# Kernel optimization log

Measured on AMD Instinct MI355X. Metric: run time of the kernel, lower is better.

Reference implementation:

```python
import math
import jax, jax.numpy as jnp
import numpy as np

EMBED_DIM = 768
NUM_HEADS = 12
HEAD_DIM = EMBED_DIM // NUM_HEADS
NUM_BUCKETS = 32
MAX_DISTANCE = 128
B, S = 8, 1024


def setup_inputs() -> dict:
    key = jax.random.key(0)
    ks = jax.random.split(key, 16)
    sc = 0.02
    d = {
        "query": jax.random.normal(ks[0], (B, S, EMBED_DIM), jnp.float32),
        "Wq": jax.random.normal(ks[1], (EMBED_DIM, EMBED_DIM), jnp.float32) * sc,
        "bq": jnp.zeros((EMBED_DIM,), jnp.float32),
        "Wk": jax.random.normal(ks[2], (EMBED_DIM, EMBED_DIM), jnp.float32) * sc,
        "bk": jnp.zeros((EMBED_DIM,), jnp.float32),
        "Wv": jax.random.normal(ks[3], (EMBED_DIM, EMBED_DIM), jnp.float32) * sc,
        "bv": jnp.zeros((EMBED_DIM,), jnp.float32),
        "Wo": jax.random.normal(ks[4], (EMBED_DIM, EMBED_DIM), jnp.float32) * sc,
        "bo": jnp.zeros((EMBED_DIM,), jnp.float32),
        "rel_embed": jax.random.normal(ks[5], (NUM_BUCKETS, NUM_HEADS), jnp.float32) * sc,
        "gru_W": jax.random.normal(ks[6], (HEAD_DIM, 8), jnp.float32) * sc,
        "gru_b": jnp.zeros((8,), jnp.float32),
        "gru_const": jnp.ones((1, NUM_HEADS, 1, 1), jnp.float32),
    }
    return d


def _rel_pos_bias(rel_embed, seq_len):
    # bidirectional T5-style bucketing, matching WavLM._relative_positions_bucket
    ctx = jnp.arange(seq_len)[:, None]
    mem = jnp.arange(seq_len)[None, :]
    rp = mem - ctx  # [S, S]
    nb = NUM_BUCKETS // 2
    buckets = (rp > 0).astype(jnp.int32) * nb
    arp = jnp.abs(rp)
    max_exact = nb // 2
    is_small = arp < max_exact
    # truncation toward zero == astype for positive values; clamp to avoid log(0)
    large = max_exact + (
        jnp.log(jnp.maximum(arp, 1).astype(jnp.float32) / max_exact)
        / math.log(MAX_DISTANCE / max_exact)
        * (nb - max_exact)
    ).astype(jnp.int32)
    large = jnp.minimum(large, nb - 1)
    buckets = buckets + jnp.where(is_small, arp, large)
    # embedding lookup -> [S, S, H] -> [H, S, S]
    return rel_embed[buckets].transpose(2, 0, 1)


def reference(query, Wq, bq, Wk, bk, Wv, bv, Wo, bo, rel_embed, gru_W, gru_b, gru_const):
    b, s, e = query.shape
    h, d = NUM_HEADS, HEAD_DIM
    pos_bias = _rel_pos_bias(rel_embed, s)  # [H, S, S]

    # GRU-style gate computed from raw query, per head
    ql = query.reshape(b, s, h, d).transpose(0, 2, 1, 3)  # [B, H, S, D]
    g = jax.nn.sigmoid((ql @ gru_W + gru_b).reshape(b, h, s, 2, 4).sum(-1))  # [B,H,S,2]
    gate_a = g[..., 0:1]
    gate_b = g[..., 1:2]
    gate = gate_a * (gate_b * gru_const - 1.0) + 2.0  # [B, H, S, 1]
    attn_mask = gate * pos_bias[None]  # [B, H, S, S]

    scale = d ** (-0.5)
    q = (query @ Wq + bq).reshape(b, s, h, d).transpose(0, 2, 1, 3) * scale
    k = (query @ Wk + bk).reshape(b, s, h, d).transpose(0, 2, 1, 3)
    v = (query @ Wv + bv).reshape(b, s, h, d).transpose(0, 2, 1, 3)

    scores = jnp.einsum("bhqd,bhkd->bhqk", q, k) + attn_mask
    w = jax.nn.softmax(scores, axis=-1)  # max-subtraction in torch is a no-op math-wise
    out = jnp.einsum("bhqk,bhkd->bhqd", w, v)
    out = out.transpose(0, 2, 1, 3).reshape(b, s, h * d)
    return out @ Wo + bo
```

## Files before the change

### kernel.cpp

```cpp
#include <hip/hip_runtime.h>
#include <hip/hip_bf16.h>
#include <math.h>

#define EMBED 768
#define NH 12
#define HD 64
#define SEQ 1024
#define BATCH 8
#define NROWS (BATCH * SEQ)
#define LOG2E 1.44269504088896340736f

typedef __attribute__((ext_vector_type(4))) float f32x4;
typedef __attribute__((ext_vector_type(8))) short short8;
typedef __attribute__((ext_vector_type(8))) _Float16 half8;
typedef unsigned short u16;

__device__ __forceinline__ u16 f2bf(float x) {
    union { float f; unsigned u; } v; v.f = x;
    unsigned r = v.u + 0x7fff + ((v.u >> 16) & 1);
    return (u16)(r >> 16);
}
__device__ __forceinline__ void split2h(float x, u16& hi, u16& lo) {
    _Float16 h = (_Float16)x;
    _Float16 l = (_Float16)(x - (float)h);
    union { _Float16 f; u16 u; } a, b;
    a.f = h; b.f = l;
    hi = a.u; lo = b.u;
}
__device__ __forceinline__ u16 f2h(float x) {
    union { _Float16 f; u16 u; } a; a.f = (_Float16)x; return a.u;
}
__device__ __forceinline__ unsigned pkbf(float a, float b) {
    union { __hip_bfloat162 v; unsigned u; } cv;
    cv.v = __float22bfloat162_rn(make_float2(a, b));
    return cv.u;
}
__device__ __forceinline__ void gll16(const void* g, void* l) {
    __builtin_amdgcn_global_load_lds(
        (const __attribute__((address_space(1))) unsigned int*)g,
        (__attribute__((address_space(3))) unsigned int*)l,
        16, 0, 0);
}

__global__ void bias_table_kernel(const float* __restrict__ rel_embed,
                                  float* __restrict__ bt)
{
    int idx = blockIdx.x * 256 + threadIdx.x;
    const int total = NH * 2047;
    if (idx >= total) return;
    int h    = idx / 2047;
    int dpos = idx - h * 2047;
    int rp   = dpos - 1023;
    int bucket = (rp > 0) ? 16 : 0;
    int arp = rp < 0 ? -rp : rp;
    if (arp < 8) {
        bucket += arp;
    } else {
        double v = log((double)arp / 8.0) / log(16.0) * 8.0;
        int l = 8 + (int)v;
        if (l > 15) l = 15;
        bucket += l;
    }
    bt[idx] = rel_embed[bucket * NH + h] * LOG2E;
}

__global__ void gate_kernel(const float* __restrict__ query,
                            const float* __restrict__ gru_W,
                            const float* __restrict__ gru_b,
                            const float* __restrict__ gru_c,
                            float* __restrict__ gate)
{
    int idx = blockIdx.x * 256 + threadIdx.x;
    if (idx >= BATCH * NH * SEQ) return;
    int s  = idx & (SEQ - 1);
    int bh = idx >> 10;
    int h  = bh % NH;
    int b  = bh / NH;

    const float* x = query + ((size_t)(b * SEQ + s) * EMBED + h * HD);
    float z[8] = {0.f, 0.f, 0.f, 0.f, 0.f, 0.f, 0.f, 0.f};
    for (int d = 0; d < HD; ++d) {
        float xv = x[d];
        const float* wrow = gru_W + d * 8;
        #pragma unroll
        for (int c = 0; c < 8; ++c) z[c] += xv * wrow[c];
    }
    float s0 = (z[0] + gru_b[0]) + (z[1] + gru_b[1]) + (z[2] + gru_b[2]) + (z[3] + gru_b[3]);
    float s1 = (z[4] + gru_b[4]) + (z[5] + gru_b[5]) + (z[6] + gru_b[6]) + (z[7] + gru_b[7]);
    float g0 = 1.f / (1.f + expf(-s0));
    float g1 = 1.f / (1.f + expf(-s1));
    gate[idx] = g0 * (g1 * gru_c[h] - 1.f) + 2.f;
}

__global__ __launch_bounds__(256)
void convertA_h(const float* __restrict__ A, u16* __restrict__ Ah,
                u16* __restrict__ Al)
{
    int idx = (blockIdx.x * 256 + threadIdx.x) * 4;
    float4 v = *(const float4*)(A + idx);
    ushort4 h, l;
    split2h(v.x, h.x, l.x); split2h(v.y, h.y, l.y);
    split2h(v.z, h.z, l.z); split2h(v.w, h.w, l.w);
    *(ushort4*)(Ah + idx) = h;
    *(ushort4*)(Al + idx) = l;
}

__global__ __launch_bounds__(256)
void convertWT_h(const float* __restrict__ W, u16* __restrict__ WT)
{
    __shared__ float tile[32][33];
    int t  = threadIdx.x;
    int k0 = blockIdx.y * 32, n0 = blockIdx.x * 32;
    int r = t >> 3, c = (t & 7) * 4;
    float4 v = *(const float4*)&W[(size_t)(k0 + r) * EMBED + n0 + c];
    tile[r][c] = v.x; tile[r][c + 1] = v.y; tile[r][c + 2] = v.z; tile[r][c + 3] = v.w;
    __syncthreads();
    int n = t >> 3, ks = (t & 7) * 4;
    ushort4 h;
    h.x = f2h(tile[ks    ][n]);
    h.y = f2h(tile[ks + 1][n]);
    h.z = f2h(tile[ks + 2][n]);
    h.w = f2h(tile[ks + 3][n]);
    *(ushort4*)&WT[(size_t)(n0 + n) * EMBED + k0 + ks] = h;
}

__global__ __launch_bounds__(256)
void gemm_qkv(const u16* __restrict__ Ah, const u16* __restrict__ Al,
              const u16* __restrict__ WqT, const u16* __restrict__ WkT,
              const u16* __restrict__ WvT,
              const float* __restrict__ bq, const float* __restrict__ bk,
              const float* __restrict__ bv,
              u16* __restrict__ Qb, u16* __restrict__ Kb, u16* __restrict__ VT,
              float qscale)
{
    __shared__ u16 Ah_s[32 * 32];
    __shared__ u16 Al_s[32 * 32];
    __shared__ u16 Bq_s[128 * 32];
    __shared__ u16 Bk_s[128 * 32];
    __shared__ u16 Bv_s[128 * 32];

    const int t    = threadIdx.x;
    const int lane = t & 63;
    const int wid  = t >> 6;
    const int L    = lane & 15;
    const int quad = lane >> 4;
    const int row0 = blockIdx.y * 32;
    const int col0 = blockIdx.x * 128;
    const int wm   = (wid >> 1) * 16;
    const int wn   = (wid & 1) * 64;

    f32x4 accQ[4], accK[4], accV[4];
    #pragma unroll
    for (int nt = 0; nt < 4; ++nt) {
        accQ[nt] = (f32x4){0.f, 0.f, 0.f, 0.f};
        accK[nt] = (f32x4){0.f, 0.f, 0.f, 0.f};
        accV[nt] = (f32x4){0.f, 0.f, 0.f, 0.f};
    }

    const int rA = (wid & 1) * 16 + (lane >> 2);
    const int cA = (lane & 3) ^ (rA & 3);
    const u16* gA = ((wid < 2) ? Ah : Al) + (size_t)(row0 + rA) * EMBED + 8 * cA;
    char* lA = (char*)((wid < 2) ? Ah_s : Al_s) + (wid & 1) * 1024;

    const int rB = t >> 2;
    const int cB = (t & 3) ^ (rB & 3);
    const size_t bo0 = (size_t)(col0 + rB) * EMBED + 8 * cB;
    const size_t bo1 = (size_t)(col0 + 64 + rB) * EMBED + 8 * cB;
    char* lBq = (char*)Bq_s + wid * 1024;
    char* lBk = (char*)Bk_s + wid * 1024;
    char* lBv = (char*)Bv_s + wid * 1024;

    const int swz = 8 * (quad ^ (L & 3));

    for (int k0 = 0; k0 < EMBED; k0 += 32) {
        __syncthreads();
        gll16(gA + k0, lA);
        gll16(WqT + bo0 + k0, lBq); gll16(WqT + bo1 + k0, lBq + 4096);
        gll16(WkT + bo0 + k0, lBk); gll16(WkT + bo1 + k0, lBk + 4096);
        gll16(WvT + bo0 + k0, lBv); gll16(WvT + bo1 + k0, lBv + 4096);
        __syncthreads();

        half8 ah = *(const half8*)&Ah_s[(wm + L) * 32 + swz];
        half8 al = *(const half8*)&Al_s[(wm + L) * 32 + swz];
        #pragma unroll
        for (int nt = 0; nt < 4; ++nt) {
            const int boff = (wn + nt * 16 + L) * 32 + swz;
            half8 b0 = *(const half8*)&Bq_s[boff];
            accQ[nt] = __builtin_amdgcn_mfma_f32_16x16x32_f16(ah, b0, accQ[nt], 0, 0, 0);
            accQ[nt] = __builtin_amdgcn_mfma_f32_16x16x32_f16(al, b0, accQ[nt], 0, 0, 0);
            half8 b1 = *(const half8*)&Bk_s[boff];
            accK[nt] = __builtin_amdgcn_mfma_f32_16x16x32_f16(ah, b1, accK[nt], 0, 0, 0);
            accK[nt] = __builtin_amdgcn_mfma_f32_16x16x32_f16(al, b1, accK[nt], 0, 0, 0);
            half8 b2 = *(const half8*)&Bv_s[boff];
            accV[nt] = __builtin_amdgcn_mfma_f32_16x16x32_f16(ah, b2, accV[nt], 0, 0, 0);
            accV[nt] = __builtin_amdgcn_mfma_f32_16x16x32_f16(al, b2, accV[nt], 0, 0, 0);
        }
    }

    float bq4[4], bk4[4], bv4[4];
    #pragma unroll
    for (int nt = 0; nt < 4; ++nt) {
        int n = col0 + wn + nt * 16 + L;
        bq4[nt] = bq[n]; bk4[nt] = bk[n]; bv4[nt] = bv[n];
    }

    const int rowa = row0 + wm + quad * 4;
    #pragma unroll
    for (int r = 0; r < 4; ++r) {
        size_t base = (size_t)(rowa + r) * EMBED + col0 + wn + L;
        #pragma unroll
        for (int nt = 0; nt < 4; ++nt) {
            Qb[base + nt * 16] = f2bf((accQ[nt][r] + bq4[nt]) * qscale);
            Kb[base + nt * 16] = f2bf(accK[nt][r] + bk4[nt]);
        }
    }
    {
        int b_  = rowa >> 10;
        int s0_ = rowa & 1023;
        #pragma unroll
        for (int nt = 0; nt < 4; ++nt) {
            int n = col0 + wn + nt * 16 + L;
            int hh = n >> 6, dd = n & 63;
            ushort4 pk;
            pk.x = f2bf(accV[nt][0] + bv4[nt]);
            pk.y = f2bf(accV[nt][1] + bv4[nt]);
            pk.z = f2bf(accV[nt][2] + bv4[nt]);
            pk.w = f2bf(accV[nt][3] + bv4[nt]);
            *(ushort4*)&VT[((size_t)(b_ * NH + hh) * HD + dd) * SEQ + s0_] = pk;
        }
    }
}

__global__ __launch_bounds__(256)
void gemm_out(const u16* __restrict__ Ah, const u16* __restrict__ Al,
              const u16* __restrict__ BT, const float* __restrict__ bias,
              float* __restrict__ C)
{
    __shared__ u16 Ah_s[32 * 32];
    __shared__ u16 Al_s[32 * 32];
    __shared__ u16 B_s[128 * 32];

    const int t    = threadIdx.x;
    const int lane = t & 63;
    const int wid  = t >> 6;
    const int L    = lane & 15;
    const int quad = lane >> 4;
    const int row0 = blockIdx.y * 32;
    const int col0 = blockIdx.x * 128;
    const int wm   = (wid >> 1) * 16;
    const int wn   = (wid & 1) * 64;

    f32x4 acc[4];
    #pragma unroll
    for (int nt = 0; nt < 4; ++nt) acc[nt] = (f32x4){0.f, 0.f, 0.f, 0.f};

    const int rA = (wid & 1) * 16 + (lane >> 2);
    const int cA = (lane & 3) ^ (rA & 3);
    const u16* gA = ((wid < 2) ? Ah : Al) + (size_t)(row0 + rA) * EMBED + 8 * cA;
    char* lA = (char*)((wid < 2) ? Ah_s : Al_s) + (wid & 1) * 1024;

    const int rB = t >> 2;
    const int cB = (t & 3) ^ (rB & 3);
    const u16* gB0 = BT + (size_t)(col0 + rB) * EMBED + 8 * cB;
    const u16* gB1 = BT + (size_t)(col0 + 64 + rB) * EMBED + 8 * cB;
    char* lB = (char*)B_s + wid * 1024;

    const int swz = 8 * (quad ^ (L & 3));

    for (int k0 = 0; k0 < EMBED; k0 += 32) {
        __syncthreads();
        gll16(gA  + k0, lA);
        gll16(gB0 + k0, lB);
        gll16(gB1 + k0, lB + 4096);
        __syncthreads();

        half8 ah = *(const half8*)&Ah_s[(wm + L) * 32 + swz];
        half8 al = *(const half8*)&Al_s[(wm + L) * 32 + swz];
        #pragma unroll
        for (int nt = 0; nt < 4; ++nt) {
            half8 b = *(const half8*)&B_s[(wn + nt * 16 + L) * 32 + swz];
            acc[nt] = __builtin_amdgcn_mfma_f32_16x16x32_f16(ah, b, acc[nt], 0, 0, 0);
            acc[nt] = __builtin_amdgcn_mfma_f32_16x16x32_f16(al, b, acc[nt], 0, 0, 0);
        }
    }

    float b4[4];
    #pragma unroll
    for (int nt = 0; nt < 4; ++nt) b4[nt] = bias[col0 + wn + nt * 16 + L];
    #pragma unroll
    for (int r = 0; r < 4; ++r) {
        size_t base = (size_t)(row0 + wm + quad * 4 + r) * EMBED + col0 + wn + L;
        #pragma unroll
        for (int nt = 0; nt < 4; ++nt)
            C[base + nt * 16] = acc[nt][r] + b4[nt];
    }
}

__global__ __launch_bounds__(256)
void attn_mfma3(const u16* __restrict__ Qg, const u16* __restrict__ Kg,
                const u16* __restrict__ VTg, const float* __restrict__ gate,
                const float* __restrict__ bias_tab,
                u16* __restrict__ Oh, u16* __restrict__ Ol)
{
    __shared__ float2   btP[2047];
    __shared__ u16      Klds[64 * 64];
    __shared__ u16      Vlds[64 * 64];
    __shared__ unsigned PB[4][32 * 20];

    const int t    = threadIdx.x;
    const int lane = t & 63;
    const int wid  = t >> 6;
    const int L    = lane & 15;
    const int quad = lane >> 4;

    const int bh = blockIdx.y;
    const int b  = bh / NH;
    const int h  = bh % NH;
    const int qw = blockIdx.x * 128 + wid * 32;

    for (int i = t; i < 2047; i += 256) {
        float a  = bias_tab[h * 2047 + i];
        float nb = (i < 2046) ? bias_tab[h * 2047 + i + 1] : 0.f;
        btP[i] = make_float2(a, nb);
    }

    short8 qf[2][2];
    int   qabs[2];
    float g2[2];
    #pragma unroll
    for (int qt = 0; qt < 2; ++qt) {
        qabs[qt] = qw + qt * 16 + L;
        g2[qt]   = gate[(size_t)bh * SEQ + qabs[qt]];
        const u16* qp = Qg + ((size_t)(b * SEQ + qabs[qt]) * EMBED + h * HD + quad * 8);
        qf[qt][0] = *(const short8*)qp;
        qf[qt][1] = *(const short8*)(qp + 32);
    }

    float lac[2] = {0.f, 0.f};
    f32x4 o[4][2];
    #pragma unroll
    for (int dt = 0; dt < 4; ++dt)
        #pragma unroll
        for (int qt = 0; qt < 2; ++qt) o[dt][qt] = (f32x4){0.f, 0.f, 0.f, 0.f};

    const int k_a = t >> 3, c_a = (t & 7) ^ (k_a & 7);
    const u16* gK0 = Kg + ((size_t)(b * SEQ + k_a) * EMBED + h * HD + 8 * c_a);
    const u16* gK1 = Kg + ((size_t)(b * SEQ + 32 + k_a) * EMBED + h * HD + 8 * c_a);
    char* lK0 = (char*)Klds + wid * 1024;
    char* lK1 = (char*)Klds + 4096 + wid * 1024;

    const int d_a = t >> 3, cv_a = (t & 7) ^ (d_a & 7);
    const u16* gV0 = VTg + ((size_t)(bh * HD + d_a) * SEQ + 8 * cv_a);
    const u16* gV1 = VTg + ((size_t)(bh * HD + 32 + d_a) * SEQ + 8 * cv_a);
    char* lV0 = (char*)Vlds + wid * 1024;
    char* lV1 = (char*)Vlds + 4096 + wid * 1024;

    unsigned* PBw = PB[wid];

    for (int k0 = 0; k0 < SEQ; k0 += 64) {
        __syncthreads();
        gll16(gK0 + (size_t)k0 * EMBED, lK0);
        gll16(gK1 + (size_t)k0 * EMBED, lK1);
        gll16(gV0 + k0, lV0);
        gll16(gV1 + k0, lV1);
        __syncthreads();

        f32x4 st[4][2];
        #pragma unroll
        for (int kt = 0; kt < 4; ++kt)
            #pragma unroll
            for (int qt = 0; qt < 2; ++qt) st[kt][qt] = (f32x4){0.f, 0.f, 0.f, 0.f};
        #pragma unroll
        for (int c = 0; c < 2; ++c) {
            #pragma unroll
            for (int kt = 0; kt < 4; ++kt) {
                int krow = kt * 16 + L;
                short8 kf = *(const short8*)&Klds[krow * 64 + 8 * ((c * 4 + quad) ^ (krow & 7))];
                st[kt][0] = __builtin_amdgcn_mfma_f32_16x16x32_bf16(kf, qf[0][c], st[kt][0], 0, 0, 0);
                st[kt][1] = __builtin_amdgcn_mfma_f32_16x16x32_bf16(kf, qf[1][c], st[kt][1], 0, 0, 0);
            }
        }

        #pragma unroll
        for (int c = 0; c < 2; ++c) {
            #pragma unroll
            for (int kt2 = 0; kt2 < 2; ++kt2) {
                int kt = c * 2 + kt2;
                #pragma unroll
                for (int qt = 0; qt < 2; ++qt) {
                    int bidx = k0 + kt * 16 + quad * 4 - qabs[qt] + 1023;
                    float2 u = btP[bidx];
                    float2 v = btP[bidx + 2];
                    float p0 = __builtin_amdgcn_exp2f(st[kt][qt][0] + g2[qt] * u.x);
                    float p1 = __builtin_amdgcn_exp2f(st[kt][qt][1] + g2[qt] * u.y);
                    float p2 = __builtin_amdgcn_exp2f(st[kt][qt][2] + g2[qt] * v.x);
                    float p3 = __builtin_amdgcn_exp2f(st[kt][qt][3] + g2[qt] * v.y);
                    lac[qt] += (p0 + p1) + (p2 + p3);
                    uint2 w;
                    w.x = pkbf(p0, p1);
                    w.y = pkbf(p2, p3);
                    *(uint2*)&PBw[(qt * 16 + L) * 20 + kt2 * 8 + quad * 2] = w;
                }
            }
            short8 pb[2];
            #pragma unroll
            for (int qt = 0; qt < 2; ++qt) {
                union { uint4 u4; short8 v; } w;
                w.u4 = *(const uint4*)&PBw[(qt * 16 + L) * 20 + quad * 4];
                pb[qt] = w.v;
            }
            #pragma unroll
            for (int dt = 0; dt < 4; ++dt) {
                int drow = dt * 16 + L;
                short8 vf = *(const short8*)&Vlds[drow * 64 + 8 * ((c * 4 + quad) ^ (drow & 7))];
                o[dt][0] = __builtin_amdgcn_mfma_f32_16x16x32_bf16(vf, pb[0], o[dt][0], 0, 0, 0);
                o[dt][1] = __builtin_amdgcn_mfma_f32_16x16x32_bf16(vf, pb[1], o[dt][1], 0, 0, 0);
            }
        }
    }

    #pragma unroll
    for (int qt = 0; qt < 2; ++qt) {
        lac[qt] += __shfl_xor(lac[qt], 16);
        lac[qt] += __shfl_xor(lac[qt], 32);
    }
    #pragma unroll
    for (int qt = 0; qt < 2; ++qt) {
        float inv = 1.f / lac[qt];
        #pragma unroll
        for (int dt = 0; dt < 4; ++dt) {
            ushort4 h4, l4;
            split2h(o[dt][qt][0] * inv, h4.x, l4.x);
            split2h(o[dt][qt][1] * inv, h4.y, l4.y);
            split2h(o[dt][qt][2] * inv, h4.z, l4.z);
            split2h(o[dt][qt][3] * inv, h4.w, l4.w);
            size_t base = (size_t)(b * SEQ + qabs[qt]) * EMBED + h * HD + dt * 16 + quad * 4;
            *(ushort4*)&Oh[base] = h4;
            *(ushort4*)&Ol[base] = l4;
        }
    }
}

extern "C" void kernel_launch(void* const* d_in, const int* in_sizes, int n_in,
                              void* d_out, int out_size, void* d_ws, size_t ws_size,
                              hipStream_t stream)
{
    (void)in_sizes; (void)n_in; (void)out_size; (void)ws_size;
    const float* query = (const float*)d_in[0];
    const float* Wq    = (const float*)d_in[1];
    const float* bq    = (const float*)d_in[2];
    const float* Wk    = (const float*)d_in[3];
    const float* bk    = (const float*)d_in[4];
    const float* Wv    = (const float*)d_in[5];
    const float* bv    = (const float*)d_in[6];
    const float* Wo    = (const float*)d_in[7];
    const float* bo    = (const float*)d_in[8];
    const float* rel   = (const float*)d_in[9];
    const float* gruW  = (const float*)d_in[10];
    const float* gruB  = (const float*)d_in[11];
    const float* gruC  = (const float*)d_in[12];
    float* out = (float*)d_out;

    const size_t NE = (size_t)NROWS * EMBED;
    const size_t WN = (size_t)EMBED * EMBED;
    u16* ws   = (u16*)d_ws;
    u16* Ah   = ws;
    u16* Al   = Ah + NE;
    u16* WqT  = Al + NE;
    u16* WkT  = WqT + WN;
    u16* WvT  = WkT + WN;
    u16* WoT  = WvT + WN;
    u16* Qb   = WoT + WN;
    u16* Kb   = Qb + NE;
    u16* VT   = Kb + NE;
    u16* Ohb  = VT + NE;
    u16* Olb  = Ohb + NE;
    float* gate = (float*)(Olb + NE);
    float* bt   = gate + (size_t)BATCH * NH * SEQ;

    bias_table_kernel<<<(NH * 2047 + 255) / 256, 256, 0, stream>>>(rel, bt);
    gate_kernel<<<(BATCH * NH * SEQ + 255) / 256, 256, 0, stream>>>(query, gruW, gruB, gruC, gate);

    convertA_h<<<NE / 1024, 256, 0, stream>>>(query, Ah, Al);
    dim3 wt(EMBED / 32, EMBED / 32);
    convertWT_h<<<wt, 256, 0, stream>>>(Wq, WqT);
    convertWT_h<<<wt, 256, 0, stream>>>(Wk, WkT);
    convertWT_h<<<wt, 256, 0, stream>>>(Wv, WvT);
    convertWT_h<<<wt, 256, 0, stream>>>(Wo, WoT);

    dim3 gq(EMBED / 128, NROWS / 32);
    gemm_qkv<<<gq, 256, 0, stream>>>(Ah, Al, WqT, WkT, WvT, bq, bk, bv,
                                     Qb, Kb, VT, 0.125f * LOG2E);

    attn_mfma3<<<dim3(SEQ / 128, BATCH * NH), 256, 0, stream>>>(Qb, Kb, VT, gate, bt, Ohb, Olb);

    gemm_out<<<gq, 256, 0, stream>>>(Ohb, Olb, WoT, bo, out);
}
```

Measured before the change: 298.1 us.

## Double-buffer GEMM B tiles, load A directly to registers, merge weight conversions

Both projection GEMMs now double-buffer the weight tiles in LDS. Each next tile is prefetched with global_load_lds while MFMAs run on the current one, and a single barrier per iteration replaces the two __syncthreads. The A operand (hi/lo halves) is read straight from global memory into registers instead of being staged in LDS. The output GEMM doubles rows per block to reuse each B tile twice, and the four weight-transpose launches are merged into one 3D launch. In exchange, LDS use and register pressure go up, the launch_bounds occupancy hint changes, and the A loads from global are uncoalesced per lane.

```diff
diff --git a/kernel.cpp b/kernel.cpp
--- a/kernel.cpp
+++ b/kernel.cpp
@@ -40,6 +40,11 @@
         (const __attribute__((address_space(1))) unsigned int*)g,
         (__attribute__((address_space(3))) unsigned int*)l,
         16, 0, 0);
+}
+__device__ __forceinline__ void pipe_barrier() {
+    asm volatile("s_waitcnt vmcnt(0)" ::: "memory");
+    __builtin_amdgcn_s_barrier();
+    asm volatile("" ::: "memory");
 }
 
 __global__ void bias_table_kernel(const float* __restrict__ rel_embed,
@@ -106,9 +111,16 @@
 }
 
 __global__ __launch_bounds__(256)
-void convertWT_h(const float* __restrict__ W, u16* __restrict__ WT)
+void convertWT4(const float* __restrict__ W0, const float* __restrict__ W1,
+                const float* __restrict__ W2, const float* __restrict__ W3,
+                u16* __restrict__ T0, u16* __restrict__ T1,
+                u16* __restrict__ T2, u16* __restrict__ T3)
 {
     __shared__ float tile[32][33];
+    const float* W = (blockIdx.z == 0) ? W0 : (blockIdx.z == 1) ? W1
+                   : (blockIdx.z == 2) ? W2 : W3;
+    u16* WT        = (blockIdx.z == 0) ? T0 : (blockIdx.z == 1) ? T1
+                   : (blockIdx.z == 2) ? T2 : T3;
     int t  = threadIdx.x;
     int k0 = blockIdx.y * 32, n0 = blockIdx.x * 32;
     int r = t >> 3, c = (t & 7) * 4;
@@ -124,20 +136,16 @@
     *(ushort4*)&WT[(size_t)(n0 + n) * EMBED + k0 + ks] = h;
 }
 
-__global__ __launch_bounds__(256)
-void gemm_qkv(const u16* __restrict__ Ah, const u16* __restrict__ Al,
-              const u16* __restrict__ WqT, const u16* __restrict__ WkT,
-              const u16* __restrict__ WvT,
-              const float* __restrict__ bq, const float* __restrict__ bk,
-              const float* __restrict__ bv,
-              u16* __restrict__ Qb, u16* __restrict__ Kb, u16* __restrict__ VT,
-              float qscale)
-{
-    __shared__ u16 Ah_s[32 * 32];
-    __shared__ u16 Al_s[32 * 32];
-    __shared__ u16 Bq_s[128 * 32];
-    __shared__ u16 Bk_s[128 * 32];
-    __shared__ u16 Bv_s[128 * 32];
+__global__ __launch_bounds__(256, 3)
+void gemm_qkv_p(const u16* __restrict__ Ah, const u16* __restrict__ Al,
+                const u16* __restrict__ WqT, const u16* __restrict__ WkT,
+                const u16* __restrict__ WvT,
+                const float* __restrict__ bq, const float* __restrict__ bk,
+                const float* __restrict__ bv,
+                u16* __restrict__ Qb, u16* __restrict__ Kb, u16* __restrict__ VT,
+                float qscale)
+{
+    __shared__ u16 Bs[2][3][128 * 32];
 
     const int t    = threadIdx.x;
     const int lane = t & 63;
@@ -157,44 +165,56 @@
         accV[nt] = (f32x4){0.f, 0.f, 0.f, 0.f};
     }
 
-    const int rA = (wid & 1) * 16 + (lane >> 2);
-    const int cA = (lane & 3) ^ (rA & 3);
-    const u16* gA = ((wid < 2) ? Ah : Al) + (size_t)(row0 + rA) * EMBED + 8 * cA;
-    char* lA = (char*)((wid < 2) ? Ah_s : Al_s) + (wid & 1) * 1024;
-
     const int rB = t >> 2;
     const int cB = (t & 3) ^ (rB & 3);
     const size_t bo0 = (size_t)(col0 + rB) * EMBED + 8 * cB;
     const size_t bo1 = (size_t)(col0 + 64 + rB) * EMBED + 8 * cB;
-    char* lBq = (char*)Bq_s + wid * 1024;
-    char* lBk = (char*)Bk_s + wid * 1024;
-    char* lBv = (char*)Bv_s + wid * 1024;
+
+    const u16* ApH = Ah + (size_t)(row0 + wm + L) * EMBED + quad * 8;
+    const u16* ApL = Al + (size_t)(row0 + wm + L) * EMBED + quad * 8;
 
     const int swz = 8 * (quad ^ (L & 3));
 
-    for (int k0 = 0; k0 < EMBED; k0 += 32) {
-        __syncthreads();
-        gll16(gA + k0, lA);
-        gll16(WqT + bo0 + k0, lBq); gll16(WqT + bo1 + k0, lBq + 4096);
-        gll16(WkT + bo0 + k0, lBk); gll16(WkT + bo1 + k0, lBk + 4096);
-        gll16(WvT + bo0 + k0, lBv); gll16(WvT + bo1 + k0, lBv + 4096);
-        __syncthreads();
-
-        half8 ah = *(const half8*)&Ah_s[(wm + L) * 32 + swz];
-        half8 al = *(const half8*)&Al_s[(wm + L) * 32 + swz];
+    {
+        char* base = (char*)Bs + wid * 1024;
+        gll16(WqT + bo0, base);             gll16(WqT + bo1, base + 4096);
+        gll16(WkT + bo0, base + 8192);      gll16(WkT + bo1, base + 12288);
+        gll16(WvT + bo0, base + 16384);     gll16(WvT + bo1, base + 20480);
+    }
+    half8 ah = *(const half8*)ApH;
+    half8 al = *(const half8*)ApL;
+
+    int cur = 0;
+    for (int k0 = 0; k0 < EMBED; k0 += 32, cur ^= 1) {
+        pipe_barrier();
+
+        half8 ahn, aln;
+        if (k0 + 32 < EMBED) {
+            char* base = (char*)Bs + (cur ^ 1) * 24576 + wid * 1024;
+            gll16(WqT + bo0 + k0 + 32, base);         gll16(WqT + bo1 + k0 + 32, base + 4096);
+            gll16(WkT + bo0 + k0 + 32, base + 8192);  gll16(WkT + bo1 + k0 + 32, base + 12288);
+            gll16(WvT + bo0 + k0 + 32, base + 16384); gll16(WvT + bo1 + k0 + 32, base + 20480);
+            ahn = *(const half8*)(ApH + k0 + 32);
+            aln = *(const half8*)(ApL + k0 + 32);
+        }
+
+        const u16* Bq = &Bs[cur][0][0];
+        const u16* Bk = &Bs[cur][1][0];
+        const u16* Bv = &Bs[cur][2][0];
         #pragma unroll
         for (int nt = 0; nt < 4; ++nt) {
             const int boff = (wn + nt * 16 + L) * 32 + swz;
-            half8 b0 = *(const half8*)&Bq_s[boff];
+            half8 b0 = *(const half8*)&Bq[boff];
             accQ[nt] = __builtin_amdgcn_mfma_f32_16x16x32_f16(ah, b0, accQ[nt], 0, 0, 0);
             accQ[nt] = __builtin_amdgcn_mfma_f32_16x16x32_f16(al, b0, accQ[nt], 0, 0, 0);
-            half8 b1 = *(const half8*)&Bk_s[boff];
+            half8 b1 = *(const half8*)&Bk[boff];
             accK[nt] = __builtin_amdgcn_mfma_f32_16x16x32_f16(ah, b1, accK[nt], 0, 0, 0);
             accK[nt] = __builtin_amdgcn_mfma_f32_16x16x32_f16(al, b1, accK[nt], 0, 0, 0);
-            half8 b2 = *(const half8*)&Bv_s[boff];
+            half8 b2 = *(const half8*)&Bv[boff];
             accV[nt] = __builtin_amdgcn_mfma_f32_16x16x32_f16(ah, b2, accV[nt], 0, 0, 0);
             accV[nt] = __builtin_amdgcn_mfma_f32_16x16x32_f16(al, b2, accV[nt], 0, 0, 0);
         }
+        ah = ahn; al = aln;
     }
 
     float bq4[4], bk4[4], bv4[4];
@@ -231,69 +251,97 @@
     }
 }
 
-__global__ __launch_bounds__(256)
-void gemm_out(const u16* __restrict__ Ah, const u16* __restrict__ Al,
-              const u16* __restrict__ BT, const float* __restrict__ bias,
-              float* __restrict__ C)
-{
-    __shared__ u16 Ah_s[32 * 32];
-    __shared__ u16 Al_s[32 * 32];
-    __shared__ u16 B_s[128 * 32];
+__global__ __launch_bounds__(256, 3)
+void gemm_out_p(const u16* __restrict__ Ah, const u16* __restrict__ Al,
+                const u16* __restrict__ BT, const float* __restrict__ bias,
+                float* __restrict__ C)
+{
+    __shared__ u16 Bs[2][128 * 32];
 
     const int t    = threadIdx.x;
     const int lane = t & 63;
     const int wid  = t >> 6;
     const int L    = lane & 15;
     const int quad = lane >> 4;
-    const int row0 = blockIdx.y * 32;
+    const int row0 = blockIdx.y * 64;
     const int col0 = blockIdx.x * 128;
-    const int wm   = (wid >> 1) * 16;
+    const int wm   = (wid >> 1) * 32;
     const int wn   = (wid & 1) * 64;
 
-    f32x4 acc[4];
-    #pragma unroll
-    for (int nt = 0; nt < 4; ++nt) acc[nt] = (f32x4){0.f, 0.f, 0.f, 0.f};
-
-    const int rA = (wid & 1) * 16 + (lane >> 2);
-    const int cA = (lane & 3) ^ (rA & 3);
-    const u16* gA = ((wid < 2) ? Ah : Al) + (size_t)(row0 + rA) * EMBED + 8 * cA;
-    char* lA = (char*)((wid < 2) ? Ah_s : Al_s) + (wid & 1) * 1024;
+    f32x4 acc[2][4];
+    #pragma unroll
+    for (int mt = 0; mt < 2; ++mt)
+        #pragma unroll
+        for (int nt = 0; nt < 4; ++nt) acc[mt][nt] = (f32x4){0.f, 0.f, 0.f, 0.f};
 
     const int rB = t >> 2;
     const int cB = (t & 3) ^ (rB & 3);
-    const u16* gB0 = BT + (size_t)(col0 + rB) * EMBED + 8 * cB;
-    const u16* gB1 = BT + (size_t)(col0 + 64 + rB) * EMBED + 8 * cB;
-    char* lB = (char*)B_s + wid * 1024;
+    const size_t bo0 = (size_t)(col0 + rB) * EMBED + 8 * cB;
+    const size_t bo1 = (size_t)(col0 + 64 + rB) * EMBED + 8 * cB;
+
+    const u16* ApH[2]; const u16* ApL[2];
+    #pragma unroll
+    for (int mt = 0; mt < 2; ++mt) {
+        ApH[mt] = Ah + (size_t)(row0 + wm + mt * 16 + L) * EMBED + quad * 8;
+        ApL[mt] = Al + (size_t)(row0 + wm + mt * 16 + L) * EMBED + quad * 8;
+    }
 
     const int swz = 8 * (quad ^ (L & 3));
 
-    for (int k0 = 0; k0 < EMBED; k0 += 32) {
-        __syncthreads();
-        gll16(gA  + k0, lA);
-        gll16(gB0 + k0, lB);
-        gll16(gB1 + k0, lB + 4096);
-        __syncthreads();
-
-        half8 ah = *(const half8*)&Ah_s[(wm + L) * 32 + swz];
-        half8 al = *(const half8*)&Al_s[(wm + L) * 32 + swz];
+    {
+        char* base = (char*)Bs + wid * 1024;
+        gll16(BT + bo0, base);
+        gll16(BT + bo1, base + 4096);
+    }
+    half8 ah[2], al[2];
+    #pragma unroll
+    for (int mt = 0; mt < 2; ++mt) {
+        ah[mt] = *(const half8*)ApH[mt];
+        al[mt] = *(const half8*)ApL[mt];
+    }
+
+    int cur = 0;
+    for (int k0 = 0; k0 < EMBED; k0 += 32, cur ^= 1) {
+        pipe_barrier();
+
+        half8 ahn[2], aln[2];
+        if (k0 + 32 < EMBED) {
+            char* base = (char*)Bs + (cur ^ 1) * 8192 + wid * 1024;
+            gll16(BT + bo0 + k0 + 32, base);
+            gll16(BT + bo1 + k0 + 32, base + 4096);
+            #pragma unroll
+            for (int mt = 0; mt < 2; ++mt) {
+                ahn[mt] = *(const half8*)(ApH[mt] + k0 + 32);
+                aln[mt] = *(const half8*)(ApL[mt] + k0 + 32);
+            }
+        }
+
+        const u16* B = &Bs[cur][0];
         #pragma unroll
         for (int nt = 0; nt < 4; ++nt) {
-            half8 b = *(const half8*)&B_s[(wn + nt * 16 + L) * 32 + swz];
-            acc[nt] = __builtin_amdgcn_mfma_f32_16x16x32_f16(ah, b, acc[nt], 0, 0, 0);
-            acc[nt] = __builtin_amdgcn_mfma_f32_16x16x32_f16(al, b, acc[nt], 0, 0, 0);
-        }
+            half8 b = *(const half8*)&B[(wn + nt * 16 + L) * 32 + swz];
+            #pragma unroll
+            for (int mt = 0; mt < 2; ++mt) {
+                acc[mt][nt] = __builtin_amdgcn_mfma_f32_16x16x32_f16(ah[mt], b, acc[mt][nt], 0, 0, 0);
+                acc[mt][nt] = __builtin_amdgcn_mfma_f32_16x16x32_f16(al[mt], b, acc[mt][nt], 0, 0, 0);
+            }
+        }
+        #pragma unroll
+        for (int mt = 0; mt < 2; ++mt) { ah[mt] = ahn[mt]; al[mt] = aln[mt]; }
     }
 
     float b4[4];
     #pragma unroll
     for (int nt = 0; nt < 4; ++nt) b4[nt] = bias[col0 + wn + nt * 16 + L];
     #pragma unroll
-    for (int r = 0; r < 4; ++r) {
-        size_t base = (size_t)(row0 + wm + quad * 4 + r) * EMBED + col0 + wn + L;
-        #pragma unroll
-        for (int nt = 0; nt < 4; ++nt)
-            C[base + nt * 16] = acc[nt][r] + b4[nt];
-    }
+    for (int mt = 0; mt < 2; ++mt)
+        #pragma unroll
+        for (int r = 0; r < 4; ++r) {
+            size_t base = (size_t)(row0 + wm + mt * 16 + quad * 4 + r) * EMBED + col0 + wn + L;
+            #pragma unroll
+            for (int nt = 0; nt < 4; ++nt)
+                C[base + nt * 16] = acc[mt][nt][r] + b4[nt];
+        }
 }
 
 __global__ __launch_bounds__(256)
@@ -482,17 +530,15 @@
     gate_kernel<<<(BATCH * NH * SEQ + 255) / 256, 256, 0, stream>>>(query, gruW, gruB, gruC, gate);
 
     convertA_h<<<NE / 1024, 256, 0, stream>>>(query, Ah, Al);
-    dim3 wt(EMBED / 32, EMBED / 32);
-    convertWT_h<<<wt, 256, 0, stream>>>(Wq, WqT);
-    convertWT_h<<<wt, 256, 0, stream>>>(Wk, WkT);
-    convertWT_h<<<wt, 256, 0, stream>>>(Wv, WvT);
-    convertWT_h<<<wt, 256, 0, stream>>>(Wo, WoT);
+    convertWT4<<<dim3(EMBED / 32, EMBED / 32, 4), 256, 0, stream>>>(
+        Wq, Wk, Wv, Wo, WqT, WkT, WvT, WoT);
 
     dim3 gq(EMBED / 128, NROWS / 32);
-    gemm_qkv<<<gq, 256, 0, stream>>>(Ah, Al, WqT, WkT, WvT, bq, bk, bv,
-                                     Qb, Kb, VT, 0.125f * LOG2E);
+    gemm_qkv_p<<<gq, 256, 0, stream>>>(Ah, Al, WqT, WkT, WvT, bq, bk, bv,
+                                       Qb, Kb, VT, 0.125f * LOG2E);
 
     attn_mfma3<<<dim3(SEQ / 128, BATCH * NH), 256, 0, stream>>>(Qb, Kb, VT, gate, bt, Ohb, Olb);
 
-    gemm_out<<<gq, 256, 0, stream>>>(Ohb, Olb, WoT, bo, out);
-}
+    dim3 go(EMBED / 128, NROWS / 64);
+    gemm_out_p<<<go, 256, 0, stream>>>(Ohb, Olb, WoT, bo, out);
+}
```

Result: no change. 302.8 us (+1.6%).
